# Kernel tuning notes

Hardware: AMD Instinct MI355X
Metric: run time of the kernel (lower is better)

## Reference

```python
import jax, jax.numpy as jnp
import numpy as np

# init hyperparameters (from init_kwargs)
KD = KH = KW = 3
SD = SH = SW = 1
PD = PH = PW = 1
DD = DH = DW = 1
GROUPS = 1
DG = 1  # deformable_groups
CIN, COUT = 32, 64


def setup_inputs() -> dict:
    key = jax.random.key(0)
    k1, k2, k3, k4, k5 = jax.random.split(key, 5)
    B, D, H, W = 2, 8, 48, 48
    K = KD * KH * KW
    x = jax.random.normal(k1, (B, CIN, D, H, W), dtype=jnp.float32)
    # 2 offset components (h, w) per deformable-group kernel tap
    offset = jax.random.normal(k2, (B, 2 * DG * K, D, H, W), dtype=jnp.float32)
    mask = jax.random.uniform(k3, (B, DG * K, D, H, W), dtype=jnp.float32)
    fan_in = CIN // GROUPS * K
    weight = jax.random.normal(k4, (COUT, CIN // GROUPS, KD, KH, KW), dtype=jnp.float32) / np.sqrt(fan_in)
    bias = jax.random.uniform(k5, (COUT,), dtype=jnp.float32, minval=-1.0, maxval=1.0) / np.sqrt(fan_in)
    return {"input": x, "offset": offset, "mask": mask, "weight": weight, "bias": bias}


def reference(input, offset, mask, weight, bias):
    x = input
    B, Cin, D, H, W = x.shape
    Cout = weight.shape[0]
    K = KD * KH * KW
    Do = (D + 2 * PD - DD * (KD - 1) - 1) // SD + 1
    Ho = (H + 2 * PH - DH * (KH - 1) - 1) // SH + 1
    Wo = (W + 2 * PW - DW * (KW - 1) - 1) // SW + 1
    Cg = Cin // DG

    kdi, khi, kwi = [a.reshape(-1) for a in jnp.meshgrid(
        jnp.arange(KD), jnp.arange(KH), jnp.arange(KW), indexing="ij")]
    # depth taps: regular (un-deformed) dilated grid -> exact integer index
    d_pos = kdi[:, None] * DD + jnp.arange(Do) * SD - PD           # [K, Do]
    valid_d = (d_pos >= 0) & (d_pos < D)
    d_idx = jnp.clip(d_pos, 0, D - 1)
    h_base = (khi[:, None] * DH + jnp.arange(Ho) * SH - PH).astype(x.dtype)  # [K, Ho]
    w_base = (kwi[:, None] * DW + jnp.arange(Wo) * SW - PW).astype(x.dtype)  # [K, Wo]

    off = offset.reshape(B, DG, K, 2, Do, Ho, Wo)
    m = mask.reshape(B, DG, K, Do, Ho, Wo)

    h = h_base[None, None, :, None, :, None] + off[:, :, :, 0]     # [B,DG,K,Do,Ho,Wo]
    w = w_base[None, None, :, None, None, :] + off[:, :, :, 1]
    h0f, w0f = jnp.floor(h), jnp.floor(w)
    lh, lw = h - h0f, w - w0f
    h0, w0 = h0f.astype(jnp.int32), w0f.astype(jnp.int32)
    h1, w1 = h0 + 1, w0 + 1

    vd = valid_d[None, None, :, :, None, None]
    inb_h = lambda hi: (hi >= 0) & (hi < H)
    inb_w = lambda wi: (wi >= 0) & (wi < W)

    xg = x.reshape(B, DG, Cg, D, H, W)

    def gather(hI, wI):
        hc = jnp.clip(hI, 0, H - 1)
        wc = jnp.clip(wI, 0, W - 1)
        def per(xi, hh, ww):  # xi [Cg,D,H,W]; hh,ww [K,Do,Ho,Wo]
            dfull = jnp.broadcast_to(d_idx[:, :, None, None], hh.shape)
            return xi[:, dfull, hh, ww]  # [Cg,K,Do,Ho,Wo]
        return jax.vmap(jax.vmap(per))(xg, hc, wc)  # [B,DG,Cg,K,Do,Ho,Wo]

    w00 = ((1 - lh) * (1 - lw) * (inb_h(h0) & inb_w(w0) & vd))[:, :, None]
    w01 = ((1 - lh) * lw * (inb_h(h0) & inb_w(w1) & vd))[:, :, None]
    w10 = (lh * (1 - lw) * (inb_h(h1) & inb_w(w0) & vd))[:, :, None]
    w11 = (lh * lw * (inb_h(h1) & inb_w(w1) & vd))[:, :, None]

    val = (gather(h0, w0) * w00 + gather(h0, w1) * w01 +
           gather(h1, w0) * w10 + gather(h1, w1) * w11)   # [B,DG,Cg,K,Do,Ho,Wo]

    sampled = (val * m[:, :, None]).reshape(B, Cin, K, Do, Ho, Wo)
    w2 = weight.reshape(Cout, Cin // GROUPS, K)  # groups == 1
    out = jnp.einsum("bckdhw,ock->bodhw", sampled, w2)
    return out + bias[None, :, None, None, None]
```

## Files before the change

kernel.cpp:

```cpp
#include <hip/hip_runtime.h>
#include <hip/hip_fp16.h>

#define BSZ 2
#define CIN 32
#define COUT 64
#define DD_ 8
#define HH_ 48
#define WW_ 48
#define KK 27
#define HWs (HH_*WW_)
#define DHW (DD_*HH_*WW_)
#define NBLK (BSZ*DD_*HH_)
#define NT 768

typedef __attribute__((ext_vector_type(8))) _Float16 half8;
typedef __attribute__((ext_vector_type(4))) float f32x4;

__device__ __forceinline__ half8 splat_h(unsigned packed, int hi) {
    union { unsigned v; _Float16 h[2]; } c; c.v = packed;
    _Float16 e = c.h[hi];
    return (half8){e, e, e, e, e, e, e, e};
}

__global__ void prep(const float* __restrict__ x, const float* __restrict__ wsrc,
                     _Float16* __restrict__ xT, _Float16* __restrict__ wf) {
    __shared__ float tile[CIN][WW_];
    int blk = blockIdx.x;
    if (blk < NBLK) {
        int h = blk % HH_;
        int t0 = blk / HH_;
        int d = t0 % DD_;
        int b = t0 / DD_;
        int base = d * HWs + h * WW_;
        for (int e = threadIdx.x; e < CIN * WW_; e += 256) {
            int ci = e / WW_, w = e - ci * WW_;
            tile[ci][w] = x[(size_t)(b * CIN + ci) * DHW + base + w];
        }
        __syncthreads();
        for (int e = threadIdx.x; e < CIN * WW_; e += 256) {
            int w = e >> 5, ci = e & 31;
            xT[(size_t)(b * DHW + base + w) * CIN + ci] = (_Float16)tile[ci][w];
        }
    } else {
        int idx = (blk - NBLK) * 256 + threadIdx.x;
        if (idx < KK * 4 * 64 * 8) {
            int j = idx & 7, l = (idx >> 3) & 63, c = (idx >> 9) & 3, k = idx >> 11;
            int co = c * 16 + (l & 15), ci = (l >> 4) * 8 + j;
            wf[idx] = (_Float16)wsrc[(co * CIN + ci) * KK + k];
        }
    }
}

template<int USE_XT>
__launch_bounds__(NT, 6)
__global__ void dcn3d(const float* __restrict__ x, const _Float16* __restrict__ xT,
                      const float* __restrict__ off, const float* __restrict__ msk,
                      const float* __restrict__ wsrc, const _Float16* __restrict__ wf,
                      const float* __restrict__ bias, float* __restrict__ out) {
    int blk = blockIdx.x;
    int h = blk % HH_;
    int t0 = blk / HH_;
    int d = t0 % DD_;
    int b = t0 / DD_;

    __shared__ uint4 Pp[KK * WW_];
    __shared__ half8 Sh[2][7 * 3 * 64];

    int tid = threadIdx.x;
    int lane = tid & 63;
    int wid = tid >> 6;
    int cstrip = wid & 3;
    int T = wid >> 2;
    int spb = d * HWs + h * WW_;

    const _Float16* xTb = xT + (size_t)b * DHW * CIN;
    const float* xb = x + (size_t)b * CIN * DHW;

    for (int p = tid; p < KK * WW_; p += NT) {
        int k = p / WW_;
        int w = p - k * WW_;
        int kd = k / 9, kh2 = (k / 3) % 3, kw2 = k % 3;
        int dpos = d + kd - 1;
        bool vd = (dpos >= 0) && (dpos < DD_);
        int didx = min(max(dpos, 0), DD_ - 1);
        int rb = didx * HWs;
        int sp = spb + w;
        float oh = off[(b * (2 * KK) + 2 * k) * DHW + sp];
        float ow = off[(b * (2 * KK) + 2 * k + 1) * DHW + sp];
        float m  = msk[(b * KK + k) * DHW + sp];
        float vm = vd ? m : 0.f;
        float hhf = (float)(kh2 + h - 1) + oh;
        float wwf = (float)(kw2 + w - 1) + ow;
        float h0f = floorf(hhf), w0f = floorf(wwf);
        float lh = hhf - h0f, lw = wwf - w0f;
        int h0 = (int)h0f, w0 = (int)w0f, h1 = h0 + 1, w1 = w0 + 1;
        bool ih0 = (h0 >= 0) && (h0 < HH_), ih1 = (h1 >= 0) && (h1 < HH_);
        bool iw0 = (w0 >= 0) && (w0 < WW_), iw1 = (w1 >= 0) && (w1 < WW_);
        int h0c = min(max(h0, 0), HH_ - 1), h1c = min(max(h1, 0), HH_ - 1);
        int w0c = min(max(w0, 0), WW_ - 1), w1c = min(max(w1, 0), WW_ - 1);
        float f00 = (ih0 && iw0) ? (1.f - lh) * (1.f - lw) * vm : 0.f;
        float f01 = (ih0 && iw1) ? (1.f - lh) * lw * vm : 0.f;
        float f10 = (ih1 && iw0) ? lh * (1.f - lw) * vm : 0.f;
        float f11 = (ih1 && iw1) ? lh * lw * vm : 0.f;
        uint4 P;
        P.x = (unsigned)(rb + h0c * WW_ + w0c) | ((unsigned)(rb + h0c * WW_ + w1c) << 16);
        P.y = (unsigned)(rb + h1c * WW_ + w0c) | ((unsigned)(rb + h1c * WW_ + w1c) << 16);
        __half2 ha = __floats2half2_rn(f00, f01);
        __half2 hb = __floats2half2_rn(f10, f11);
        P.z = *(const unsigned*)&ha;
        P.w = *(const unsigned*)&hb;
        Pp[p] = P;
    }
    __syncthreads();

    half8 qA00 = {}, qA01 = {}, qA10 = {}, qA11 = {};
    half8 qB00 = {}, qB01 = {}, qB10 = {}, qB11 = {};
    unsigned wzA = 0, wwA = 0, wzB = 0, wwB = 0;
    int sbA = 0, sbB = 0;
    bool vB = false;

#define TASK(S, T_, KB)                                                          \
    {                                                                            \
        int t = (T_);                                                            \
        int p = t >> 2, g = t & 3;                                               \
        int kl = p / WW_, w = p - kl * WW_;                                      \
        uint4 P = Pp[((KB) + kl) * WW_ + w];                                     \
        wz##S = P.z; ww##S = P.w;                                                \
        sb##S = (kl * 3 + (w >> 4)) * 64 + g * 16 + (w & 15);                    \
        if (USE_XT) {                                                            \
            const _Float16* bp = xTb + g * 8;                                    \
            q##S##00 = *(const half8*)(bp + ((size_t)(P.x & 0xFFFFu) << 5));     \
            q##S##01 = *(const half8*)(bp + ((size_t)(P.x >> 16) << 5));         \
            q##S##10 = *(const half8*)(bp + ((size_t)(P.y & 0xFFFFu) << 5));     \
            q##S##11 = *(const half8*)(bp + ((size_t)(P.y >> 16) << 5));         \
        } else {                                                                 \
            _Pragma("unroll")                                                    \
            for (int j = 0; j < 8; ++j) {                                        \
                const float* xp = xb + (size_t)(g * 8 + j) * DHW;                \
                q##S##00[j] = (_Float16)xp[P.x & 0xFFFFu];                       \
                q##S##01[j] = (_Float16)xp[P.x >> 16];                           \
                q##S##10[j] = (_Float16)xp[P.y & 0xFFFFu];                       \
                q##S##11[j] = (_Float16)xp[P.y >> 16];                           \
            }                                                                    \
        }                                                                        \
    }

#define ISSUE(NKg, KB)                                                           \
    TASK(A, tid, KB)                                                             \
    vB = tid < (NKg) * 192 - NT;                                                 \
    if (vB) TASK(B, tid + NT, KB)

#define WRITE(BUF)                                                               \
    Sh[BUF][sbA] = qA00 * splat_h(wzA, 0) + qA01 * splat_h(wzA, 1)               \
                 + qA10 * splat_h(wwA, 0) + qA11 * splat_h(wwA, 1);              \
    if (vB)                                                                      \
        Sh[BUF][sbB] = qB00 * splat_h(wzB, 0) + qB01 * splat_h(wzB, 1)           \
                     + qB10 * splat_h(wwB, 0) + qB11 * splat_h(wwB, 1);

    f32x4 acc = {0.f, 0.f, 0.f, 0.f};

#define GEMM(NKg, KB, BUF)                                                       \
    _Pragma("unroll")                                                            \
    for (int kl = 0; kl < (NKg); ++kl) {                                         \
        half8 a;                                                                 \
        if (USE_XT) {                                                            \
            a = *(const half8*)(wf + ((((KB) + kl) * 4 + cstrip) * 64 + lane) * 8); \
        } else {                                                                 \
            int co = cstrip * 16 + (lane & 15);                                  \
            int ci0 = (lane >> 4) * 8;                                           \
            _Pragma("unroll")                                                    \
            for (int j = 0; j < 8; ++j)                                          \
                a[j] = (_Float16)wsrc[(co * CIN + ci0 + j) * KK + (KB) + kl];    \
        }                                                                        \
        half8 bfr = Sh[BUF][(kl * 3 + T) * 64 + (lane >> 4) * 16 + (lane & 15)]; \
        acc = __builtin_amdgcn_mfma_f32_16x16x32_f16(a, bfr, acc, 0, 0, 0);      \
    }

    ISSUE(7, 0)
    WRITE(0)
    __syncthreads();

    ISSUE(7, 7)
    GEMM(7, 0, 0)
    WRITE(1)
    __syncthreads();

    ISSUE(7, 14)
    GEMM(7, 7, 1)
    WRITE(0)
    __syncthreads();

    ISSUE(6, 21)
    GEMM(7, 14, 0)
    WRITE(1)
    __syncthreads();

    GEMM(6, 21, 1)

#undef TASK
#undef ISSUE
#undef WRITE
#undef GEMM

    int co0 = cstrip * 16 + (lane >> 4) * 4;
    int wcol = T * 16 + (lane & 15);
#pragma unroll
    for (int r = 0; r < 4; ++r)
        out[((b * COUT + co0 + r) * DD_ + d) * HWs + h * WW_ + wcol] = acc[r] + bias[co0 + r];
}

extern "C" void kernel_launch(void* const* d_in, const int* in_sizes, int n_in,
                              void* d_out, int out_size, void* d_ws, size_t ws_size,
                              hipStream_t stream) {
    const float* x    = (const float*)d_in[0];
    const float* off  = (const float*)d_in[1];
    const float* msk  = (const float*)d_in[2];
    const float* w    = (const float*)d_in[3];
    const float* bias = (const float*)d_in[4];
    float* out = (float*)d_out;

    const size_t XT_OFF   = 131072;
    const size_t XT_BYTES = (size_t)BSZ * DHW * CIN * sizeof(_Float16);

    _Float16* wf = (_Float16*)d_ws;
    _Float16* xT = (_Float16*)((char*)d_ws + XT_OFF);
    int use = (ws_size >= XT_OFF + XT_BYTES) ? 1 : 0;

    if (use) {
        int wblocks = (KK * 4 * 64 * 8 + 255) / 256;
        prep<<<NBLK + wblocks, 256, 0, stream>>>(x, w, xT, wf);
        dcn3d<1><<<NBLK, NT, 0, stream>>>(x, xT, off, msk, w, wf, bias, out);
    } else {
        dcn3d<0><<<NBLK, NT, 0, stream>>>(x, xT, off, msk, w, wf, bias, out);
    }
}
```

Measured before the change: 34.98 us.

## Deepen gather/GEMM pipeline to 4-tap stages with triple-buffered LDS

The 27 kernel taps are now split into 7 stages of 4 taps instead of 4 stages of 7. Each thread handles one gather task per stage instead of up to two. Gathers are issued two stages ahead using two register sets (A/B), and three shared-memory buffers let loads, bilinear combine writes and MFMA GEMM overlap. The aim is to hide global-gather latency better and cut LDS footprint, which may raise occupancy. The cost is more __syncthreads barriers and more pipeline stages.

```diff
diff --git a/kernel.cpp b/kernel.cpp
--- a/kernel.cpp
+++ b/kernel.cpp
@@ -64,7 +64,7 @@
     int b = t0 / DD_;
 
     __shared__ uint4 Pp[KK * WW_];
-    __shared__ half8 Sh[2][7 * 3 * 64];
+    __shared__ half8 Sh[3][4 * 3 * 64];
 
     int tid = threadIdx.x;
     int lane = tid & 63;
@@ -117,12 +117,10 @@
     half8 qB00 = {}, qB01 = {}, qB10 = {}, qB11 = {};
     unsigned wzA = 0, wwA = 0, wzB = 0, wwB = 0;
     int sbA = 0, sbB = 0;
-    bool vB = false;
-
-#define TASK(S, T_, KB)                                                          \
-    {                                                                            \
-        int t = (T_);                                                            \
-        int p = t >> 2, g = t & 3;                                               \
+
+#define ISSUE(S, KB, NKg)                                                        \
+    if ((NKg) == 4 || tid < (NKg) * 192) {                                       \
+        int p = tid >> 2, g = tid & 3;                                           \
         int kl = p / WW_, w = p - kl * WW_;                                      \
         uint4 P = Pp[((KB) + kl) * WW_ + w];                                     \
         wz##S = P.z; ww##S = P.w;                                                \
@@ -145,17 +143,10 @@
         }                                                                        \
     }
 
-#define ISSUE(NKg, KB)                                                           \
-    TASK(A, tid, KB)                                                             \
-    vB = tid < (NKg) * 192 - NT;                                                 \
-    if (vB) TASK(B, tid + NT, KB)
-
-#define WRITE(BUF)                                                               \
-    Sh[BUF][sbA] = qA00 * splat_h(wzA, 0) + qA01 * splat_h(wzA, 1)               \
-                 + qA10 * splat_h(wwA, 0) + qA11 * splat_h(wwA, 1);              \
-    if (vB)                                                                      \
-        Sh[BUF][sbB] = qB00 * splat_h(wzB, 0) + qB01 * splat_h(wzB, 1)           \
-                     + qB10 * splat_h(wwB, 0) + qB11 * splat_h(wwB, 1);
+#define WRITE(S, BUF, NKg)                                                       \
+    if ((NKg) == 4 || tid < (NKg) * 192)                                         \
+        Sh[BUF][sb##S] = q##S##00 * splat_h(wz##S, 0) + q##S##01 * splat_h(wz##S, 1) \
+                       + q##S##10 * splat_h(ww##S, 0) + q##S##11 * splat_h(ww##S, 1);
 
     f32x4 acc = {0.f, 0.f, 0.f, 0.f};
 
@@ -176,28 +167,42 @@
         acc = __builtin_amdgcn_mfma_f32_16x16x32_f16(a, bfr, acc, 0, 0, 0);      \
     }
 
-    ISSUE(7, 0)
-    WRITE(0)
-    __syncthreads();
-
-    ISSUE(7, 7)
-    GEMM(7, 0, 0)
-    WRITE(1)
-    __syncthreads();
-
-    ISSUE(7, 14)
-    GEMM(7, 7, 1)
-    WRITE(0)
-    __syncthreads();
-
-    ISSUE(6, 21)
-    GEMM(7, 14, 0)
-    WRITE(1)
-    __syncthreads();
-
-    GEMM(6, 21, 1)
-
-#undef TASK
+    ISSUE(A, 0, 4)
+    ISSUE(B, 4, 4)
+    WRITE(A, 0, 4)
+    __syncthreads();
+
+    ISSUE(A, 8, 4)
+    GEMM(4, 0, 0)
+    WRITE(B, 1, 4)
+    __syncthreads();
+
+    ISSUE(B, 12, 4)
+    GEMM(4, 4, 1)
+    WRITE(A, 2, 4)
+    __syncthreads();
+
+    ISSUE(A, 16, 4)
+    GEMM(4, 8, 2)
+    WRITE(B, 0, 4)
+    __syncthreads();
+
+    ISSUE(B, 20, 4)
+    GEMM(4, 12, 0)
+    WRITE(A, 1, 4)
+    __syncthreads();
+
+    ISSUE(A, 24, 3)
+    GEMM(4, 16, 1)
+    WRITE(B, 2, 4)
+    __syncthreads();
+
+    GEMM(4, 20, 2)
+    WRITE(A, 0, 3)
+    __syncthreads();
+
+    GEMM(3, 24, 0)
+
 #undef ISSUE
 #undef WRITE
 #undef GEMM
```

Result: slower. 39.54 us (+13.0%).

## Restructure DCN kernel to per-wave register sampling with software-pipelined gathers

Applied to the files above, without the earlier changes.

The main kernel shrinks from 768 to 192 threads per block. Each wave now owns 16 output columns and computes all 64 output channels with four MFMA accumulators. It builds the bilinear-sampled B fragment directly in registers, so the shared-memory staging buffer and its per-stage barriers are gone. Gathers are software-pipelined three taps deep to hide global latency. In exchange, each block has far fewer waves, the per-block offset preprocessing runs with fewer threads, and register pressure rises. The fallback path becomes a simple scalar reference kernel.

```diff
diff --git a/kernel.cpp b/kernel.cpp
--- a/kernel.cpp
+++ b/kernel.cpp
@@ -11,7 +11,6 @@
 #define HWs (HH_*WW_)
 #define DHW (DD_*HH_*WW_)
 #define NBLK (BSZ*DD_*HH_)
-#define NT 768
 
 typedef __attribute__((ext_vector_type(8))) _Float16 half8;
 typedef __attribute__((ext_vector_type(4))) float f32x4;
@@ -51,11 +50,10 @@
     }
 }
 
-template<int USE_XT>
-__launch_bounds__(NT, 6)
-__global__ void dcn3d(const float* __restrict__ x, const _Float16* __restrict__ xT,
+__launch_bounds__(192, 3)
+__global__ void dcn3d(const _Float16* __restrict__ xT,
                       const float* __restrict__ off, const float* __restrict__ msk,
-                      const float* __restrict__ wsrc, const _Float16* __restrict__ wf,
+                      const _Float16* __restrict__ wf,
                       const float* __restrict__ bias, float* __restrict__ out) {
     int blk = blockIdx.x;
     int h = blk % HH_;
@@ -64,19 +62,15 @@
     int b = t0 / DD_;
 
     __shared__ uint4 Pp[KK * WW_];
-    __shared__ half8 Sh[2][7 * 3 * 64];
 
     int tid = threadIdx.x;
     int lane = tid & 63;
-    int wid = tid >> 6;
-    int cstrip = wid & 3;
-    int T = wid >> 2;
+    int T = tid >> 6;
+    int wl = lane & 15;
+    int g = lane >> 4;
     int spb = d * HWs + h * WW_;
 
-    const _Float16* xTb = xT + (size_t)b * DHW * CIN;
-    const float* xb = x + (size_t)b * CIN * DHW;
-
-    for (int p = tid; p < KK * WW_; p += NT) {
+    for (int p = tid; p < KK * WW_; p += 192) {
         int k = p / WW_;
         int w = p - k * WW_;
         int kd = k / 9, kh2 = (k / 3) % 3, kw2 = k % 3;
@@ -113,100 +107,110 @@
     }
     __syncthreads();
 
-    half8 qA00 = {}, qA01 = {}, qA10 = {}, qA11 = {};
-    half8 qB00 = {}, qB01 = {}, qB10 = {}, qB11 = {};
-    unsigned wzA = 0, wwA = 0, wzB = 0, wwB = 0;
-    int sbA = 0, sbB = 0;
-    bool vB = false;
-
-#define TASK(S, T_, KB)                                                          \
-    {                                                                            \
-        int t = (T_);                                                            \
-        int p = t >> 2, g = t & 3;                                               \
-        int kl = p / WW_, w = p - kl * WW_;                                      \
-        uint4 P = Pp[((KB) + kl) * WW_ + w];                                     \
-        wz##S = P.z; ww##S = P.w;                                                \
-        sb##S = (kl * 3 + (w >> 4)) * 64 + g * 16 + (w & 15);                    \
-        if (USE_XT) {                                                            \
-            const _Float16* bp = xTb + g * 8;                                    \
-            q##S##00 = *(const half8*)(bp + ((size_t)(P.x & 0xFFFFu) << 5));     \
-            q##S##01 = *(const half8*)(bp + ((size_t)(P.x >> 16) << 5));         \
-            q##S##10 = *(const half8*)(bp + ((size_t)(P.y & 0xFFFFu) << 5));     \
-            q##S##11 = *(const half8*)(bp + ((size_t)(P.y >> 16) << 5));         \
-        } else {                                                                 \
-            _Pragma("unroll")                                                    \
-            for (int j = 0; j < 8; ++j) {                                        \
-                const float* xp = xb + (size_t)(g * 8 + j) * DHW;                \
-                q##S##00[j] = (_Float16)xp[P.x & 0xFFFFu];                       \
-                q##S##01[j] = (_Float16)xp[P.x >> 16];                           \
-                q##S##10[j] = (_Float16)xp[P.y & 0xFFFFu];                       \
-                q##S##11[j] = (_Float16)xp[P.y >> 16];                           \
-            }                                                                    \
-        }                                                                        \
-    }
-
-#define ISSUE(NKg, KB)                                                           \
-    TASK(A, tid, KB)                                                             \
-    vB = tid < (NKg) * 192 - NT;                                                 \
-    if (vB) TASK(B, tid + NT, KB)
-
-#define WRITE(BUF)                                                               \
-    Sh[BUF][sbA] = qA00 * splat_h(wzA, 0) + qA01 * splat_h(wzA, 1)               \
-                 + qA10 * splat_h(wwA, 0) + qA11 * splat_h(wwA, 1);              \
-    if (vB)                                                                      \
-        Sh[BUF][sbB] = qB00 * splat_h(wzB, 0) + qB01 * splat_h(wzB, 1)           \
-                     + qB10 * splat_h(wwB, 0) + qB11 * splat_h(wwB, 1);
-
-    f32x4 acc = {0.f, 0.f, 0.f, 0.f};
-
-#define GEMM(NKg, KB, BUF)                                                       \
-    _Pragma("unroll")                                                            \
-    for (int kl = 0; kl < (NKg); ++kl) {                                         \
-        half8 a;                                                                 \
-        if (USE_XT) {                                                            \
-            a = *(const half8*)(wf + ((((KB) + kl) * 4 + cstrip) * 64 + lane) * 8); \
-        } else {                                                                 \
-            int co = cstrip * 16 + (lane & 15);                                  \
-            int ci0 = (lane >> 4) * 8;                                           \
-            _Pragma("unroll")                                                    \
-            for (int j = 0; j < 8; ++j)                                          \
-                a[j] = (_Float16)wsrc[(co * CIN + ci0 + j) * KK + (KB) + kl];    \
-        }                                                                        \
-        half8 bfr = Sh[BUF][(kl * 3 + T) * 64 + (lane >> 4) * 16 + (lane & 15)]; \
-        acc = __builtin_amdgcn_mfma_f32_16x16x32_f16(a, bfr, acc, 0, 0, 0);      \
-    }
-
-    ISSUE(7, 0)
-    WRITE(0)
-    __syncthreads();
-
-    ISSUE(7, 7)
-    GEMM(7, 0, 0)
-    WRITE(1)
-    __syncthreads();
-
-    ISSUE(7, 14)
-    GEMM(7, 7, 1)
-    WRITE(0)
-    __syncthreads();
-
-    ISSUE(6, 21)
-    GEMM(7, 14, 0)
-    WRITE(1)
-    __syncthreads();
-
-    GEMM(6, 21, 1)
-
-#undef TASK
-#undef ISSUE
-#undef WRITE
-#undef GEMM
-
-    int co0 = cstrip * 16 + (lane >> 4) * 4;
+    const _Float16* bp = xT + (size_t)b * DHW * CIN + g * 8;
+    int pbase = T * 16 + wl;
+
+    f32x4 acc0 = {0.f, 0.f, 0.f, 0.f};
+    f32x4 acc1 = acc0, acc2 = acc0, acc3 = acc0;
+
+    uint4 P0, P1, P2;
+    half8 c0_00, c0_01, c0_10, c0_11;
+    half8 c1_00, c1_01, c1_10, c1_11;
+    half8 c2_00, c2_01, c2_10, c2_11;
+
+#define PREAD(S, K) P##S = Pp[(K) * WW_ + pbase];
+#define CISSUE(S) { \
+    c##S##_00 = *(const half8*)(bp + ((size_t)(P##S.x & 0xFFFFu) << 5)); \
+    c##S##_01 = *(const half8*)(bp + ((size_t)(P##S.x >> 16) << 5)); \
+    c##S##_10 = *(const half8*)(bp + ((size_t)(P##S.y & 0xFFFFu) << 5)); \
+    c##S##_11 = *(const half8*)(bp + ((size_t)(P##S.y >> 16) << 5)); }
+#define COMP(S, K) { \
+    const _Float16* wp = wf + (size_t)(K) * 2048 + lane * 8; \
+    half8 a0 = *(const half8*)(wp); \
+    half8 a1 = *(const half8*)(wp + 512); \
+    half8 a2 = *(const half8*)(wp + 1024); \
+    half8 a3 = *(const half8*)(wp + 1536); \
+    half8 bf = c##S##_00 * splat_h(P##S.z, 0) + c##S##_01 * splat_h(P##S.z, 1) \
+             + c##S##_10 * splat_h(P##S.w, 0) + c##S##_11 * splat_h(P##S.w, 1); \
+    acc0 = __builtin_amdgcn_mfma_f32_16x16x32_f16(a0, bf, acc0, 0, 0, 0); \
+    acc1 = __builtin_amdgcn_mfma_f32_16x16x32_f16(a1, bf, acc1, 0, 0, 0); \
+    acc2 = __builtin_amdgcn_mfma_f32_16x16x32_f16(a2, bf, acc2, 0, 0, 0); \
+    acc3 = __builtin_amdgcn_mfma_f32_16x16x32_f16(a3, bf, acc3, 0, 0, 0); }
+#define STEP(J, CUR, NX2) CISSUE(NX2) COMP(CUR, J) PREAD(CUR, (J) + 3)
+
+    PREAD(0, 0) PREAD(1, 1) PREAD(2, 2)
+    CISSUE(0) CISSUE(1)
+
+    STEP(0, 0, 2)  STEP(1, 1, 0)  STEP(2, 2, 1)
+    STEP(3, 0, 2)  STEP(4, 1, 0)  STEP(5, 2, 1)
+    STEP(6, 0, 2)  STEP(7, 1, 0)  STEP(8, 2, 1)
+    STEP(9, 0, 2)  STEP(10, 1, 0) STEP(11, 2, 1)
+    STEP(12, 0, 2) STEP(13, 1, 0) STEP(14, 2, 1)
+    STEP(15, 0, 2) STEP(16, 1, 0) STEP(17, 2, 1)
+    STEP(18, 0, 2) STEP(19, 1, 0) STEP(20, 2, 1)
+    STEP(21, 0, 2) STEP(22, 1, 0) STEP(23, 2, 1)
+    CISSUE(2) COMP(0, 24)
+    COMP(1, 25)
+    COMP(2, 26)
+
+#undef PREAD
+#undef CISSUE
+#undef COMP
+#undef STEP
+
+    int rg = (lane >> 4) * 4;
     int wcol = T * 16 + (lane & 15);
-#pragma unroll
-    for (int r = 0; r < 4; ++r)
-        out[((b * COUT + co0 + r) * DD_ + d) * HWs + h * WW_ + wcol] = acc[r] + bias[co0 + r];
+    int obase = (b * COUT * DD_ + d) * HWs + h * WW_ + wcol;
+#define ST(C, ACC)                                                         \
+    _Pragma("unroll")                                                      \
+    for (int r = 0; r < 4; ++r)                                            \
+        out[obase + ((C) * 16 + rg + r) * DHW] = ACC[r] + bias[(C) * 16 + rg + r];
+    ST(0, acc0) ST(1, acc1) ST(2, acc2) ST(3, acc3)
+#undef ST
+}
+
+__global__ void dcn3d_ref(const float* __restrict__ x, const float* __restrict__ off,
+                          const float* __restrict__ msk, const float* __restrict__ w,
+                          const float* __restrict__ bias, float* __restrict__ out) {
+    int blk = blockIdx.x;
+    int h = blk % HH_;
+    int t0 = blk / HH_;
+    int d = t0 % DD_;
+    int b = t0 / DD_;
+    for (int e = threadIdx.x; e < COUT * WW_; e += 256) {
+        int co = e / WW_, wo = e - co * WW_;
+        float acc = bias[co];
+        for (int k = 0; k < KK; ++k) {
+            int kd = k / 9, kh2 = (k / 3) % 3, kw2 = k % 3;
+            int dpos = d + kd - 1;
+            if (dpos < 0 || dpos >= DD_) continue;
+            int sp = d * HWs + h * WW_ + wo;
+            float oh = off[(b * (2 * KK) + 2 * k) * DHW + sp];
+            float ow = off[(b * (2 * KK) + 2 * k + 1) * DHW + sp];
+            float m  = msk[(b * KK + k) * DHW + sp];
+            float hhf = (float)(kh2 + h - 1) + oh;
+            float wwf = (float)(kw2 + wo - 1) + ow;
+            float h0f = floorf(hhf), w0f = floorf(wwf);
+            float lh = hhf - h0f, lw = wwf - w0f;
+            int h0 = (int)h0f, w0 = (int)w0f, h1 = h0 + 1, w1 = w0 + 1;
+            bool ih0 = (h0 >= 0) && (h0 < HH_), ih1 = (h1 >= 0) && (h1 < HH_);
+            bool iw0 = (w0 >= 0) && (w0 < WW_), iw1 = (w1 >= 0) && (w1 < WW_);
+            int h0c = min(max(h0, 0), HH_ - 1), h1c = min(max(h1, 0), HH_ - 1);
+            int w0c = min(max(w0, 0), WW_ - 1), w1c = min(max(w1, 0), WW_ - 1);
+            float f00 = (ih0 && iw0) ? (1.f - lh) * (1.f - lw) * m : 0.f;
+            float f01 = (ih0 && iw1) ? (1.f - lh) * lw * m : 0.f;
+            float f10 = (ih1 && iw0) ? lh * (1.f - lw) * m : 0.f;
+            float f11 = (ih1 && iw1) ? lh * lw * m : 0.f;
+            int rb = dpos * HWs;
+            for (int ci = 0; ci < CIN; ++ci) {
+                const float* xp = x + (size_t)(b * CIN + ci) * DHW;
+                float v = f00 * xp[rb + h0c * WW_ + w0c] + f01 * xp[rb + h0c * WW_ + w1c]
+                        + f10 * xp[rb + h1c * WW_ + w0c] + f11 * xp[rb + h1c * WW_ + w1c];
+                acc += w[(co * CIN + ci) * KK + k] * v;
+            }
+        }
+        out[((b * COUT + co) * DD_ + d) * HWs + h * WW_ + wo] = acc;
+    }
 }
 
 extern "C" void kernel_launch(void* const* d_in, const int* in_sizes, int n_in,
@@ -229,8 +233,8 @@
     if (use) {
         int wblocks = (KK * 4 * 64 * 8 + 255) / 256;
         prep<<<NBLK + wblocks, 256, 0, stream>>>(x, w, xT, wf);
-        dcn3d<1><<<NBLK, NT, 0, stream>>>(x, xT, off, msk, w, wf, bias, out);
+        dcn3d<<<NBLK, 192, 0, stream>>>(xT, off, msk, wf, bias, out);
     } else {
-        dcn3d<0><<<NBLK, NT, 0, stream>>>(x, xT, off, msk, w, wf, bias, out);
-    }
-}
+        dcn3d_ref<<<NBLK, 256, 0, stream>>>(x, off, msk, w, bias, out);
+    }
+}
```

Measured after the change: 42.76 us. 22.2% more time.
